# Performance work log

Measured on AMD Instinct MI355X. Metric: run time of the kernel, lower is better.

The kernel has to match this reference:

```python
import jax, jax.numpy as jnp
import numpy as np

IN_DIM = 128
SLOT_SIZE = 64
NUM_SLOTS = 8
NUM_ITERS = 3
MLP_HDIM = 128
EPSILON = 1e-08


def _layernorm(x, g, b, eps=1e-5):
    m = jnp.mean(x, axis=-1, keepdims=True)
    v = jnp.mean((x - m) ** 2, axis=-1, keepdims=True)
    return (x - m) * jax.lax.rsqrt(v + eps) * g + b


def setup_inputs() -> dict:
    key = jax.random.key(0)
    ks = jax.random.split(key, 16)
    H, D, K, M = SLOT_SIZE, IN_DIM, NUM_SLOTS, MLP_HDIM
    x = jax.random.normal(ks[0], (32, 4096, D), dtype=jnp.float32)
    noise = jax.random.normal(ks[1], (32, K, H), dtype=jnp.float32)
    s = lambda k, shape, fan_in: jax.random.normal(k, shape, jnp.float32) * (1.0 / np.sqrt(fan_in))
    return {
        'x': x,
        'noise': noise,
        'Wq': s(ks[2], (H, H), H),            # project_q (no bias)
        'Wk': s(ks[3], (H, D), D),            # project_k
        'Wv': s(ks[4], (H, D), D),            # project_v
        'ln_in_g': jnp.ones((D,), jnp.float32), 'ln_in_b': jnp.zeros((D,), jnp.float32),
        'ln_sl_g': jnp.ones((H,), jnp.float32), 'ln_sl_b': jnp.zeros((H,), jnp.float32),
        'ln_mlp_g': jnp.ones((H,), jnp.float32), 'ln_mlp_b': jnp.zeros((H,), jnp.float32),
        'gru_w_ih': s(ks[5], (3 * H, H), H),  # PyTorch GRUCell weight_ih (r,z,n)
        'gru_w_hh': s(ks[6], (3 * H, H), H),
        'gru_b_ih': jnp.zeros((3 * H,), jnp.float32),
        'gru_b_hh': jnp.zeros((3 * H,), jnp.float32),
        'mlp_w1': s(ks[7], (M, H), H), 'mlp_b1': jnp.zeros((M,), jnp.float32),
        'mlp_w2': s(ks[8], (H, M), M), 'mlp_b2': jnp.zeros((H,), jnp.float32),
        'slots_mu': jnp.tile(jnp.linspace(-1.0, 1.0, K, dtype=jnp.float32)[None, :, None], (1, 1, H)),
        'slots_logsigma': jnp.full((1, K, H), -1.0, dtype=jnp.float32),
    }


def reference(x, noise, Wq, Wk, Wv, ln_in_g, ln_in_b, ln_sl_g, ln_sl_b,
              ln_mlp_g, ln_mlp_b, gru_w_ih, gru_w_hh, gru_b_ih, gru_b_hh,
              mlp_w1, mlp_b1, mlp_w2, mlp_b2, slots_mu, slots_logsigma):
    B = x.shape[0]
    H, K = SLOT_SIZE, NUM_SLOTS
    xn = _layernorm(x, ln_in_g, ln_in_b)
    k = jnp.einsum('bnd,hd->bnh', xn, Wk)  # [B,N,H]
    v = jnp.einsum('bnd,hd->bnh', xn, Wv)

    scale = jax.nn.softplus(slots_logsigma) + 1e-05
    slots = slots_mu + scale * noise  # rsample, broadcast over batch -> [B,K,H]

    def step(slots):
        slots_prev = slots
        s = _layernorm(slots, ln_sl_g, ln_sl_b)
        q = jnp.einsum('bkh,gh->bkg', s, Wq)  # [B,K,H]
        scores = (H ** -0.5) * jnp.einsum('bnh,bkh->bnk', k, q)
        attn = jax.nn.softmax(scores, axis=-1) + EPSILON  # softmax over slots
        attn = attn / jnp.sum(attn, axis=1, keepdims=True)  # normalize over inputs
        updates = jnp.einsum('bnk,bnh->bkh', attn, v)
        # PyTorch GRUCell: gates ordered (r, z, n)
        u = updates.reshape(-1, H)
        h = slots_prev.reshape(-1, H)
        gx = u @ gru_w_ih.T + gru_b_ih
        gh = h @ gru_w_hh.T + gru_b_hh
        xr, xz, xn_ = jnp.split(gx, 3, axis=-1)
        hr, hz, hn = jnp.split(gh, 3, axis=-1)
        r = jax.nn.sigmoid(xr + hr)
        z = jax.nn.sigmoid(xz + hz)
        n = jnp.tanh(xn_ + r * hn)
        slots = ((1.0 - z) * n + z * h).reshape(B, K, H)
        slots = _layernorm(slots, ln_mlp_g, ln_mlp_b)
        mlp_out = jax.nn.relu(slots @ mlp_w1.T + mlp_b1) @ mlp_w2.T + mlp_b2
        return slots + mlp_out

    for _ in range(NUM_ITERS):
        slots = step(slots)
    return slots
```

## Files before the change

### kernel.cpp

```cpp
#include <hip/hip_runtime.h>

typedef __attribute__((ext_vector_type(8))) short s16x8;
typedef __attribute__((ext_vector_type(4))) float f32x4;

#define DEV static __device__ __forceinline__

DEV float b2f(unsigned short u){
  unsigned int i = ((unsigned int)u) << 16;
  float f; __builtin_memcpy(&f, &i, 4); return f;
}
DEV unsigned short f2b(float f){
  unsigned int i; __builtin_memcpy(&i, &f, 4);
  i = i + 0x7fffu + ((i >> 16) & 1u);
  return (unsigned short)(i >> 16);
}
DEV f32x4 mfma16(s16x8 a, s16x8 b, f32x4 c){
  return __builtin_amdgcn_mfma_f32_16x16x32_bf16(a, b, c, 0, 0, 0);
}
DEV s16x8 ld8f(const float* p){
  const float4* q4 = (const float4*)p;
  float4 a = q4[0], b = q4[1];
  s16x8 r;
  r[0]=(short)f2b(a.x); r[1]=(short)f2b(a.y); r[2]=(short)f2b(a.z); r[3]=(short)f2b(a.w);
  r[4]=(short)f2b(b.x); r[5]=(short)f2b(b.y); r[6]=(short)f2b(b.z); r[7]=(short)f2b(b.w);
  return r;
}

template<int C> DEV float dpp_addstep(float x){
  int y = __builtin_amdgcn_update_dpp(0, __builtin_bit_cast(int, x), C, 0xF, 0xF, true);
  return x + __builtin_bit_cast(float, y);
}
DEV float rsum16(float v){
  v = dpp_addstep<0xB1>(v);
  v = dpp_addstep<0x4E>(v);
  v = dpp_addstep<0x141>(v);
  v = dpp_addstep<0x140>(v);
  return v;
}

__global__ __launch_bounds__(256) void k_wpack(
    const float* __restrict__ Wk, const float* __restrict__ Wv,
    const float* __restrict__ wih, const float* __restrict__ whh,
    const float* __restrict__ w1, const float* __restrict__ w2,
    const float* __restrict__ Wq,
    unsigned short* __restrict__ wkb, unsigned short* __restrict__ wvb,
    unsigned short* __restrict__ wall)
{
  int t = blockIdx.x * 256 + threadIdx.x;
  int off = t * 4;
  const float* src; unsigned short* dst;
  if      (off <  8192){ src = Wk  + off;         dst = wkb  + off; }
  else if (off < 16384){ src = Wv  + off -  8192; dst = wvb  + off - 8192; }
  else if (off < 28672){ src = wih + off - 16384; dst = wall + off - 16384; }
  else if (off < 40960){ src = whh + off - 28672; dst = wall + off - 16384; }
  else if (off < 49152){ src = w1  + off - 40960; dst = wall + off - 16384; }
  else if (off < 57344){ src = w2  + off - 49152; dst = wall + off - 16384; }
  else                 { src = Wq  + off - 57344; dst = wall + off - 16384; }
  float4 v = *(const float4*)src;
  ushort4 o;
  o.x = f2b(v.x); o.y = f2b(v.y); o.z = f2b(v.z); o.w = f2b(v.w);
  *(ushort4*)dst = o;
}

__global__ __launch_bounds__(256, 4) void k_lnkv(
    const float* __restrict__ x,
    const unsigned short* __restrict__ wkb,
    const unsigned short* __restrict__ wvb,
    const float* __restrict__ lg,
    const float* __restrict__ lb,
    unsigned short* __restrict__ kg,
    unsigned short* __restrict__ vt)
{
  __shared__ unsigned int xs[128 * 68];
  const int tid = threadIdx.x;
  const int w = tid >> 6, ln = tid & 63;
  const int m16 = ln & 15, q = ln >> 4;
  const int b = blockIdx.x >> 5;
  const int nbase = (blockIdx.x & 31) << 7;
  const long rowg0 = (long)b * 4096 + nbase;

  {
    const int c = m16;
    const float4 gA = *(const float4*)(lg + c*4);
    const float4 gB = *(const float4*)(lg + 64 + c*4);
    const float4 bA = *(const float4*)(lb + c*4);
    const float4 bB = *(const float4*)(lb + 64 + c*4);
    const float* base = x + (rowg0 + w*32 + q)*128;

    float4 va[2], vb[2];
    va[0] = *(const float4*)(base + c*4);
    vb[0] = *(const float4*)(base + 64 + c*4);
    #pragma unroll
    for (int p = 0; p < 8; ++p){
      const int cur = p & 1, nxt = cur ^ 1;
      if (p < 7){
        va[nxt] = *(const float4*)(base + (p+1)*512 + c*4);
        vb[nxt] = *(const float4*)(base + (p+1)*512 + 64 + c*4);
      }
      float4 u = va[cur], t = vb[cur];
      float s1 = (u.x + u.y) + (u.z + u.w) + (t.x + t.y) + (t.z + t.w);
      float s2 = (u.x*u.x + u.y*u.y) + (u.z*u.z + u.w*u.w)
               + (t.x*t.x + t.y*t.y) + (t.z*t.z + t.w*t.w);
      s1 = rsum16(s1);
      s2 = rsum16(s2);
      float mean = s1 * (1.f/128.f);
      float var  = s2 * (1.f/128.f) - mean*mean;
      float rs = rsqrtf(var + 1e-5f);
      float y0 = (u.x - mean)*rs*gA.x + bA.x;
      float y1 = (u.y - mean)*rs*gA.y + bA.y;
      float y2 = (u.z - mean)*rs*gA.z + bA.z;
      float y3 = (u.w - mean)*rs*gA.w + bA.w;
      float y4 = (t.x - mean)*rs*gB.x + bB.x;
      float y5 = (t.y - mean)*rs*gB.y + bB.y;
      float y6 = (t.z - mean)*rs*gB.z + bB.z;
      float y7 = (t.w - mean)*rs*gB.w + bB.w;
      uint2 pkA, pkB;
      pkA.x = (unsigned int)f2b(y0) | ((unsigned int)f2b(y1) << 16);
      pkA.y = (unsigned int)f2b(y2) | ((unsigned int)f2b(y3) << 16);
      pkB.x = (unsigned int)f2b(y4) | ((unsigned int)f2b(y5) << 16);
      pkB.y = (unsigned int)f2b(y6) | ((unsigned int)f2b(y7) << 16);
      const int r = w*32 + p*4 + q;
      *(uint2*)&xs[r*68 + c*2] = pkA;
      *(uint2*)&xs[r*68 + 32 + c*2] = pkB;
    }
  }

  s16x8 bw[4][4];
  #pragma unroll
  for (int t = 0; t < 4; ++t)
    #pragma unroll
    for (int kb = 0; kb < 4; ++kb)
      bw[kb][t] = *(const s16x8*)(wkb + (t*16 + m16)*128 + kb*32 + q*8);

  __syncthreads();

  const f32x4 zf = {0.f, 0.f, 0.f, 0.f};

  #pragma unroll
  for (int mi = 0; mi < 2; ++mi){
    int n0 = (w*2 + mi) * 16;
    f32x4 acc[4];
    #pragma unroll
    for (int t = 0; t < 4; ++t) acc[t] = zf;
    #pragma unroll
    for (int kb = 0; kb < 4; ++kb){
      s16x8 af = *(const s16x8*)((const unsigned short*)(xs + (n0 + m16)*68) + kb*32 + q*8);
      #pragma unroll
      for (int t = 0; t < 4; ++t)
        acc[t] = mfma16(af, bw[kb][t], acc[t]);
    }
    #pragma unroll
    for (int t = 0; t < 4; ++t){
      int h = t*16 + m16;
      #pragma unroll
      for (int rr = 0; rr < 4; ++rr){
        long n = rowg0 + n0 + q*4 + rr;
        kg[n*64 + h] = f2b(acc[t][rr]);
      }
    }
  }

  #pragma unroll
  for (int t = 0; t < 4; ++t)
    #pragma unroll
    for (int kb = 0; kb < 4; ++kb)
      bw[kb][t] = *(const s16x8*)(wvb + (t*16 + m16)*128 + kb*32 + q*8);

  #pragma unroll
  for (int mi = 0; mi < 2; ++mi){
    int n0 = (w*2 + mi) * 16;
    f32x4 acc[4];
    #pragma unroll
    for (int t = 0; t < 4; ++t) acc[t] = zf;
    #pragma unroll
    for (int kb = 0; kb < 4; ++kb){
      s16x8 af = *(const s16x8*)((const unsigned short*)(xs + (n0 + m16)*68) + kb*32 + q*8);
      #pragma unroll
      for (int t = 0; t < 4; ++t)
        acc[t] = mfma16(af, bw[kb][t], acc[t]);
    }
    #pragma unroll
    for (int t = 0; t < 4; ++t){
      int h = t*16 + m16;
      unsigned int p0 = (unsigned int)f2b(acc[t][0]) | ((unsigned int)f2b(acc[t][1]) << 16);
      unsigned int p1 = (unsigned int)f2b(acc[t][2]) | ((unsigned int)f2b(acc[t][3]) << 16);
      uint2 pv; pv.x = p0; pv.y = p1;
      long off = ((long)b*64 + h)*4096 + nbase + n0 + q*4;
      *(uint2*)(vt + off) = pv;
    }
  }
}

__global__ __launch_bounds__(256) void k_init2(
    const float* __restrict__ noise,
    const float* __restrict__ mu,
    const float* __restrict__ lsg,
    const float* __restrict__ gsl,
    const float* __restrict__ bsl,
    const float* __restrict__ Wq,
    float* __restrict__ slots,
    unsigned short* __restrict__ qws,
    float* __restrict__ U0, float* __restrict__ U1, float* __restrict__ U2,
    float* __restrict__ S0, float* __restrict__ S1, float* __restrict__ S2)
{
  __shared__ unsigned short st[16*72];
  __shared__ __align__(16) float redS[16][4];
  __shared__ __align__(16) float redQ[16][4];
  const int tid = threadIdx.x;
  const int w = tid >> 6, ln = tid & 63;
  const int m16 = ln & 15, q = ln >> 4;
  const int r0 = blockIdx.x * 16;
  const int cw = w*16 + m16;

  float sl[4], s1[4], s2[4];
  #pragma unroll
  for (int rr = 0; rr < 4; ++rr){
    int row = r0 + q*4 + rr;
    int k = row & 7;
    float v = mu[k*64 + cw] + (log1pf(expf(lsg[k*64 + cw])) + 1e-5f) * noise[row*64 + cw];
    sl[rr] = v;
    slots[row*64 + cw] = v;
    s1[rr] = v; s2[rr] = v*v;
  }
  #pragma unroll
  for (int m = 1; m < 16; m <<= 1){
    #pragma unroll
    for (int rr = 0; rr < 4; ++rr){
      s1[rr] += __shfl_xor(s1[rr], m);
      s2[rr] += __shfl_xor(s2[rr], m);
    }
  }
  if (m16 == 0){
    #pragma unroll
    for (int rr = 0; rr < 4; ++rr){ redS[q*4+rr][w] = s1[rr]; redQ[q*4+rr][w] = s2[rr]; }
  }
  __syncthreads();
  {
    const float gs = gsl[cw], bs = bsl[cw];
    #pragma unroll
    for (int rr = 0; rr < 4; ++rr){
      f32x4 aS = *(const f32x4*)redS[q*4+rr];
      f32x4 aQ = *(const f32x4*)redQ[q*4+rr];
      float tS = aS[0]+aS[1]+aS[2]+aS[3];
      float tQ = aQ[0]+aQ[1]+aQ[2]+aQ[3];
      float mean = tS*(1.f/64.f);
      float var  = tQ*(1.f/64.f) - mean*mean;
      float rs = rsqrtf(var + 1e-5f);
      float sq = (sl[rr] - mean)*rs*gs + bs;
      st[(q*4+rr)*72 + cw] = f2b(sq);
    }
  }
  __syncthreads();
  {
    f32x4 acc = {0,0,0,0};
    #pragma unroll
    for (int ks = 0; ks < 2; ++ks){
      s16x8 a = *(const s16x8*)(st + m16*72 + ks*32 + q*8);
      acc = mfma16(a, ld8f(Wq + cw*64 + ks*32 + q*8), acc);
    }
    #pragma unroll
    for (int rr = 0; rr < 4; ++rr){
      int row = r0 + q*4 + rr;
      int bb_ = row >> 3, kk = row & 7;
      qws[(bb_*16 + kk)*64 + cw] = f2b(acc[rr] * 0.125f);
    }
  }
  {
    f32x4 z = {0,0,0,0};
    *(f32x4*)(U0 + r0*64 + tid*4) = z;
    *(f32x4*)(U1 + r0*64 + tid*4) = z;
    *(f32x4*)(U2 + r0*64 + tid*4) = z;
    if (tid < 16){ S0[r0 + tid] = 0.f; S1[r0 + tid] = 0.f; S2[r0 + tid] = 0.f; }
    int b0 = blockIdx.x * 2;
    ((unsigned int*)(qws + (b0*16 + 8)*64))[tid] = 0u;
    ((unsigned int*)(qws + ((b0+1)*16 + 8)*64))[tid] = 0u;
  }
}

__global__ __launch_bounds__(256) void k_attn2(
    const unsigned short* __restrict__ kg,
    const unsigned short* __restrict__ vt,
    const unsigned short* __restrict__ qws,
    const unsigned short* __restrict__ wall,
    const float* __restrict__ bih, const float* __restrict__ bhh,
    const float* __restrict__ b1p, const float* __restrict__ b2p,
    const float* __restrict__ gmlp, const float* __restrict__ bmlp,
    const float* __restrict__ gsl, const float* __restrict__ bsl,
    const float* __restrict__ Uin, const float* __restrict__ Sin,
    float* __restrict__ Uout, float* __restrict__ Sout,
    const float* __restrict__ slin, float* __restrict__ slout,
    int it)
{
  __shared__ float sc[256*17];
  __shared__ unsigned short aT[16*264];
  __shared__ unsigned short ut[16*72], ht[16*72], st[16*72], hid[16*136];
  __shared__ unsigned short qloc[16*72];
  __shared__ __align__(16) float redS[16][4];
  __shared__ __align__(16) float redQ[16][4];

  const int tid = threadIdx.x;
  const int w = tid >> 6, ln = tid & 63;
  const int m16 = ln & 15, q = ln >> 4;
  const int b = blockIdx.x >> 4;
  const int nbase = (blockIdx.x & 15) << 8;

  for (int i = tid; i < 8*264; i += 256) aT[8*264 + i] = 0;
  if (tid < 128){
    int row = 8 + (tid >> 4), c = (tid & 15)*4;
    ushort4 z4 = {0,0,0,0};
    *(ushort4*)&qloc[row*72 + c] = z4;
  }

  if (it == 0){
    if (tid < 128){
      int row = tid >> 4, c = (tid & 15)*4;
      *(ushort4*)&qloc[row*72 + c] = *(const ushort4*)(qws + (b*16 + row)*64 + c);
    }
  } else {
    const int r0 = (b >> 1) * 16;
    const int cw = w*16 + m16;
    const unsigned short* wihb = wall;
    const unsigned short* whhb = wall + 12288;
    const unsigned short* w1b  = wall + 24576;
    const unsigned short* w2b  = wall + 32768;
    const unsigned short* wqb  = wall + 40960;

    #pragma unroll
    for (int p = 0; p < 4; ++p){
      int row = p*4 + w;
      float sv = Sin[r0 + row];
      float uu = Uin[(r0 + row)*64 + ln] / sv;
      ut[row*72 + ln] = f2b(uu);
      ht[row*72 + ln] = f2b(slin[(r0 + row)*64 + ln]);
    }
    __syncthreads();

    f32x4 axr = {0,0,0,0}, axz = {0,0,0,0}, axn = {0,0,0,0};
    f32x4 ahr = {0,0,0,0}, ahz = {0,0,0,0}, ahn = {0,0,0,0};
    #pragma unroll
    for (int ks = 0; ks < 2; ++ks){
      s16x8 au = *(const s16x8*)(ut + m16*72 + ks*32 + q*8);
      s16x8 ah = *(const s16x8*)(ht + m16*72 + ks*32 + q*8);
      axr = mfma16(au, *(const s16x8*)(wihb + (      cw)*64 + ks*32 + q*8), axr);
      axz = mfma16(au, *(const s16x8*)(wihb + ( 64 + cw)*64 + ks*32 + q*8), axz);
      axn = mfma16(au, *(const s16x8*)(wihb + (128 + cw)*64 + ks*32 + q*8), axn);
      ahr = mfma16(ah, *(const s16x8*)(whhb + (      cw)*64 + ks*32 + q*8), ahr);
      ahz = mfma16(ah, *(const s16x8*)(whhb + ( 64 + cw)*64 + ks*32 + q*8), ahz);
      ahn = mfma16(ah, *(const s16x8*)(whhb + (128 + cw)*64 + ks*32 + q*8), ahn);
    }
    const float bxr = bih[cw], bxz = bih[64+cw], bxn = bih[128+cw];
    const float bhr = bhh[cw], bhz = bhh[64+cw], bhn = bhh[128+cw];
    float sp[4];
    #pragma unroll
    for (int rr = 0; rr < 4; ++rr){
      float xr = axr[rr] + bxr, xz = axz[rr] + bxz, xnv = axn[rr] + bxn;
      float hr = ahr[rr] + bhr, hz = ahz[rr] + bhz, hn = ahn[rr] + bhn;
      float rg = 1.f / (1.f + expf(-(xr + hr)));
      float zg = 1.f / (1.f + expf(-(xz + hz)));
      float ng = tanhf(xnv + rg*hn);
      float hv = b2f(ht[(q*4 + rr)*72 + cw]);
      sp[rr] = (1.f - zg)*ng + zg*hv;
    }

    float s1[4], s2[4];
    #pragma unroll
    for (int rr = 0; rr < 4; ++rr){ s1[rr] = sp[rr]; s2[rr] = sp[rr]*sp[rr]; }
    #pragma unroll
    for (int m = 1; m < 16; m <<= 1){
      #pragma unroll
      for (int rr = 0; rr < 4; ++rr){
        s1[rr] += __shfl_xor(s1[rr], m);
        s2[rr] += __shfl_xor(s2[rr], m);
      }
    }
    if (m16 == 0){
      #pragma unroll
      for (int rr = 0; rr < 4; ++rr){ redS[q*4+rr][w] = s1[rr]; redQ[q*4+rr][w] = s2[rr]; }
    }
    __syncthreads();
    float sl_[4];
    {
      const float gm = gmlp[cw], bm = bmlp[cw];
      #pragma unroll
      for (int rr = 0; rr < 4; ++rr){
        f32x4 aS = *(const f32x4*)redS[q*4+rr];
        f32x4 aQ = *(const f32x4*)redQ[q*4+rr];
        float tS = aS[0]+aS[1]+aS[2]+aS[3];
        float tQ = aQ[0]+aQ[1]+aQ[2]+aQ[3];
        float mean = tS*(1.f/64.f);
        float var  = tQ*(1.f/64.f) - mean*mean;
        float rs = rsqrtf(var + 1e-5f);
        sl_[rr] = (sp[rr] - mean)*rs*gm + bm;
        st[(q*4+rr)*72 + cw] = f2b(sl_[rr]);
      }
    }
    __syncthreads();

    #pragma unroll
    for (int t2 = 0; t2 < 2; ++t2){
      int nt = w*2 + t2;
      int col = nt*16 + m16;
      f32x4 acc = {0,0,0,0};
      #pragma unroll
      for (int ks = 0; ks < 2; ++ks){
        s16x8 a = *(const s16x8*)(st + m16*72 + ks*32 + q*8);
        acc = mfma16(a, *(const s16x8*)(w1b + col*64 + ks*32 + q*8), acc);
      }
      float bb = b1p[col];
      #pragma unroll
      for (int rr = 0; rr < 4; ++rr)
        hid[(q*4+rr)*136 + col] = f2b(fmaxf(acc[rr] + bb, 0.f));
    }
    __syncthreads();

    float snew[4];
    {
      f32x4 acc = {0,0,0,0};
      #pragma unroll
      for (int ks = 0; ks < 4; ++ks){
        s16x8 a = *(const s16x8*)(hid + m16*136 + ks*32 + q*8);
        acc = mfma16(a, *(const s16x8*)(w2b + cw*128 + ks*32 + q*8), acc);
      }
      float bb = b2p[cw];
      #pragma unroll
      for (int rr = 0; rr < 4; ++rr){
        snew[rr] = sl_[rr] + acc[rr] + bb;
        if ((blockIdx.x & 31) == 0)
          slout[(r0 + q*4 + rr)*64 + cw] = snew[rr];
      }
    }

    #pragma unroll
    for (int rr = 0; rr < 4; ++rr){ s1[rr] = snew[rr]; s2[rr] = snew[rr]*snew[rr]; }
    #pragma unroll
    for (int m = 1; m < 16; m <<= 1){
      #pragma unroll
      for (int rr = 0; rr < 4; ++rr){
        s1[rr] += __shfl_xor(s1[rr], m);
        s2[rr] += __shfl_xor(s2[rr], m);
      }
    }
    __syncthreads();
    if (m16 == 0){
      #pragma unroll
      for (int rr = 0; rr < 4; ++rr){ redS[q*4+rr][w] = s1[rr]; redQ[q*4+rr][w] = s2[rr]; }
    }
    __syncthreads();
    {
      const float gs = gsl[cw], bs = bsl[cw];
      #pragma unroll
      for (int rr = 0; rr < 4; ++rr){
        f32x4 aS = *(const f32x4*)redS[q*4+rr];
        f32x4 aQ = *(const f32x4*)redQ[q*4+rr];
        float tS = aS[0]+aS[1]+aS[2]+aS[3];
        float tQ = aQ[0]+aQ[1]+aQ[2]+aQ[3];
        float mean = tS*(1.f/64.f);
        float var  = tQ*(1.f/64.f) - mean*mean;
        float rs = rsqrtf(var + 1e-5f);
        float sq = (snew[rr] - mean)*rs*gs + bs;
        st[(q*4+rr)*72 + cw] = f2b(sq);
      }
    }
    __syncthreads();
    {
      f32x4 acc = {0,0,0,0};
      #pragma unroll
      for (int ks = 0; ks < 2; ++ks){
        s16x8 a = *(const s16x8*)(st + m16*72 + ks*32 + q*8);
        acc = mfma16(a, *(const s16x8*)(wqb + cw*64 + ks*32 + q*8), acc);
      }
      #pragma unroll
      for (int rr = 0; rr < 4; ++rr){
        int rloc = q*4 + rr;
        if ((rloc >> 3) == (b & 1))
          qloc[(rloc & 7)*72 + cw] = f2b(acc[rr] * 0.125f);
      }
    }
  }
  __syncthreads();

  s16x8 bq[2];
  #pragma unroll
  for (int ks = 0; ks < 2; ++ks)
    bq[ks] = *(const s16x8*)(qloc + m16*72 + ks*32 + q*8);

  #pragma unroll
  for (int mi = 0; mi < 4; ++mi){
    int n0 = (w*4 + mi)*16;
    f32x4 acc = {0.f, 0.f, 0.f, 0.f};
    #pragma unroll
    for (int ks = 0; ks < 2; ++ks){
      s16x8 af = *(const s16x8*)(kg + ((long)b*4096 + nbase + n0 + m16)*64 + ks*32 + q*8);
      acc = mfma16(af, bq[ks], acc);
    }
    #pragma unroll
    for (int rr = 0; rr < 4; ++rr)
      sc[(n0 + q*4 + rr)*17 + m16] = acc[rr];
  }
  __syncthreads();

  {
    int r = tid;
    float a8[8];
    float mx = -1e30f;
    #pragma unroll
    for (int j = 0; j < 8; ++j){ a8[j] = sc[r*17 + j]; mx = fmaxf(mx, a8[j]); }
    float ssum = 0.f;
    #pragma unroll
    for (int j = 0; j < 8; ++j){ a8[j] = expf(a8[j] - mx); ssum += a8[j]; }
    float inv = 1.f/ssum;
    #pragma unroll
    for (int j = 0; j < 8; ++j)
      aT[j*264 + r] = f2b(a8[j]*inv + 1e-8f);
  }
  __syncthreads();

  {
    int j = tid >> 5, c = tid & 31;
    float p = 0.f;
    #pragma unroll
    for (int i = 0; i < 8; ++i) p += b2f(aT[j*264 + c + 32*i]);
    #pragma unroll
    for (int m = 16; m >= 1; m >>= 1) p += __shfl_xor(p, m);
    if ((ln & 31) == 0) atomicAdd(&Sout[b*8 + j], p);
  }

  {
    f32x4 acc = {0.f, 0.f, 0.f, 0.f};
    #pragma unroll
    for (int ks = 0; ks < 8; ++ks){
      s16x8 af = *(const s16x8*)(aT + m16*264 + ks*32 + q*8);
      s16x8 bf = *(const s16x8*)(vt + ((long)b*64 + w*16 + m16)*4096 + nbase + ks*32 + q*8);
      acc = mfma16(af, bf, acc);
    }
    #pragma unroll
    for (int rr = 0; rr < 4; ++rr){
      int slot = q*4 + rr;
      if (slot < 8)
        atomicAdd(&Uout[b*512 + slot*64 + w*16 + m16], acc[rr]);
    }
  }
}

__global__ __launch_bounds__(256) void k_gru(
    const float* __restrict__ U, const float* __restrict__ S,
    float* __restrict__ slots,
    const float* __restrict__ wih, const float* __restrict__ whh,
    const float* __restrict__ bih, const float* __restrict__ bhh,
    const float* __restrict__ w1, const float* __restrict__ b1p,
    const float* __restrict__ w2, const float* __restrict__ b2p,
    const float* __restrict__ gmlp, const float* __restrict__ bmlp,
    float* __restrict__ outp)
{
  __shared__ unsigned short ut[16*72], ht[16*72], st[16*72], hid[16*136];
  __shared__ __align__(16) float redS[16][4];
  __shared__ __align__(16) float redQ[16][4];
  const int tid = threadIdx.x;
  const int w = tid >> 6, ln = tid & 63;
  const int m16 = ln & 15, q = ln >> 4;
  const int r0 = blockIdx.x * 16;
  const int cw = w*16 + m16;

  #pragma unroll
  for (int p = 0; p < 4; ++p){
    int row = p*4 + w;
    float sv = S[r0 + row];
    float uu = U[(r0 + row)*64 + ln] / sv;
    ut[row*72 + ln] = f2b(uu);
    ht[row*72 + ln] = f2b(slots[(r0 + row)*64 + ln]);
  }
  __syncthreads();

  f32x4 axr = {0,0,0,0}, axz = {0,0,0,0}, axn = {0,0,0,0};
  f32x4 ahr = {0,0,0,0}, ahz = {0,0,0,0}, ahn = {0,0,0,0};
  #pragma unroll
  for (int ks = 0; ks < 2; ++ks){
    s16x8 au = *(const s16x8*)(ut + m16*72 + ks*32 + q*8);
    s16x8 ah = *(const s16x8*)(ht + m16*72 + ks*32 + q*8);
    axr = mfma16(au, ld8f(wih + (      cw)*64 + ks*32 + q*8), axr);
    axz = mfma16(au, ld8f(wih + ( 64 + cw)*64 + ks*32 + q*8), axz);
    axn = mfma16(au, ld8f(wih + (128 + cw)*64 + ks*32 + q*8), axn);
    ahr = mfma16(ah, ld8f(whh + (      cw)*64 + ks*32 + q*8), ahr);
    ahz = mfma16(ah, ld8f(whh + ( 64 + cw)*64 + ks*32 + q*8), ahz);
    ahn = mfma16(ah, ld8f(whh + (128 + cw)*64 + ks*32 + q*8), ahn);
  }
  const float bxr = bih[cw], bxz = bih[64+cw], bxn = bih[128+cw];
  const float bhr = bhh[cw], bhz = bhh[64+cw], bhn = bhh[128+cw];
  float sp[4];
  #pragma unroll
  for (int rr = 0; rr < 4; ++rr){
    float xr = axr[rr] + bxr, xz = axz[rr] + bxz, xnv = axn[rr] + bxn;
    float hr = ahr[rr] + bhr, hz = ahz[rr] + bhz, hn = ahn[rr] + bhn;
    float rg = 1.f / (1.f + expf(-(xr + hr)));
    float zg = 1.f / (1.f + expf(-(xz + hz)));
    float ng = tanhf(xnv + rg*hn);
    float hv = b2f(ht[(q*4 + rr)*72 + cw]);
    sp[rr] = (1.f - zg)*ng + zg*hv;
  }

  float s1[4], s2[4];
  #pragma unroll
  for (int rr = 0; rr < 4; ++rr){ s1[rr] = sp[rr]; s2[rr] = sp[rr]*sp[rr]; }
  #pragma unroll
  for (int m = 1; m < 16; m <<= 1){
    #pragma unroll
    for (int rr = 0; rr < 4; ++rr){
      s1[rr] += __shfl_xor(s1[rr], m);
      s2[rr] += __shfl_xor(s2[rr], m);
    }
  }
  if (m16 == 0){
    #pragma unroll
    for (int rr = 0; rr < 4; ++rr){ redS[q*4+rr][w] = s1[rr]; redQ[q*4+rr][w] = s2[rr]; }
  }
  __syncthreads();
  float sl_[4];
  {
    const float gm = gmlp[cw], bm = bmlp[cw];
    #pragma unroll
    for (int rr = 0; rr < 4; ++rr){
      f32x4 aS = *(const f32x4*)redS[q*4+rr];
      f32x4 aQ = *(const f32x4*)redQ[q*4+rr];
      float tS = aS[0]+aS[1]+aS[2]+aS[3];
      float tQ = aQ[0]+aQ[1]+aQ[2]+aQ[3];
      float mean = tS*(1.f/64.f);
      float var  = tQ*(1.f/64.f) - mean*mean;
      float rs = rsqrtf(var + 1e-5f);
      sl_[rr] = (sp[rr] - mean)*rs*gm + bm;
      st[(q*4+rr)*72 + cw] = f2b(sl_[rr]);
    }
  }
  __syncthreads();

  #pragma unroll
  for (int t2 = 0; t2 < 2; ++t2){
    int nt = w*2 + t2;
    int col = nt*16 + m16;
    f32x4 acc = {0,0,0,0};
    #pragma unroll
    for (int ks = 0; ks < 2; ++ks){
      s16x8 a = *(const s16x8*)(st + m16*72 + ks*32 + q*8);
      acc = mfma16(a, ld8f(w1 + col*64 + ks*32 + q*8), acc);
    }
    float bb = b1p[col];
    #pragma unroll
    for (int rr = 0; rr < 4; ++rr)
      hid[(q*4+rr)*136 + col] = f2b(fmaxf(acc[rr] + bb, 0.f));
  }
  __syncthreads();

  {
    f32x4 acc = {0,0,0,0};
    #pragma unroll
    for (int ks = 0; ks < 4; ++ks){
      s16x8 a = *(const s16x8*)(hid + m16*136 + ks*32 + q*8);
      acc = mfma16(a, ld8f(w2 + cw*128 + ks*32 + q*8), acc);
    }
    float bb = b2p[cw];
    #pragma unroll
    for (int rr = 0; rr < 4; ++rr){
      int row = r0 + q*4 + rr;
      outp[row*64 + cw] = sl_[rr] + acc[rr] + bb;
    }
  }
}

extern "C" void kernel_launch(void* const* d_in, const int* in_sizes, int n_in,
                              void* d_out, int out_size, void* d_ws, size_t ws_size,
                              hipStream_t stream)
{
  const float* x    = (const float*)d_in[0];
  const float* noise= (const float*)d_in[1];
  const float* Wq   = (const float*)d_in[2];
  const float* Wk   = (const float*)d_in[3];
  const float* Wv   = (const float*)d_in[4];
  const float* ling = (const float*)d_in[5];
  const float* linb = (const float*)d_in[6];
  const float* gsl  = (const float*)d_in[7];
  const float* bsl  = (const float*)d_in[8];
  const float* gmlp = (const float*)d_in[9];
  const float* bmlp = (const float*)d_in[10];
  const float* wih  = (const float*)d_in[11];
  const float* whh  = (const float*)d_in[12];
  const float* bih  = (const float*)d_in[13];
  const float* bhh  = (const float*)d_in[14];
  const float* w1   = (const float*)d_in[15];
  const float* b1p  = (const float*)d_in[16];
  const float* w2   = (const float*)d_in[17];
  const float* b2p  = (const float*)d_in[18];
  const float* mu   = (const float*)d_in[19];
  const float* lsg  = (const float*)d_in[20];

  char* ws = (char*)d_ws;
  unsigned short* kg   = (unsigned short*)(ws);
  unsigned short* vt   = (unsigned short*)(ws + 16777216);
  char* base = ws + 33554432;
  unsigned short* qws  = (unsigned short*)(base);
  float* slotsA        = (float*)(base + 65536);
  float* slotsB        = (float*)(base + 131072);
  float* slotsC        = (float*)(base + 196608);
  float* U0            = (float*)(base + 262144);
  float* U1            = (float*)(base + 327680);
  float* U2            = (float*)(base + 393216);
  float* S0            = (float*)(base + 458752);
  float* S1            = (float*)(base + 459776);
  float* S2            = (float*)(base + 460800);
  unsigned short* wkb  = (unsigned short*)(base + 461824);
  unsigned short* wvb  = (unsigned short*)(base + 478208);
  unsigned short* wall = (unsigned short*)(base + 494592);
  float* outp          = (float*)d_out;

  hipLaunchKernelGGL(k_wpack, dim3(60), dim3(256), 0, stream,
                     Wk, Wv, wih, whh, w1, w2, Wq, wkb, wvb, wall);
  hipLaunchKernelGGL(k_lnkv, dim3(1024), dim3(256), 0, stream, x, wkb, wvb, ling, linb, kg, vt);
  hipLaunchKernelGGL(k_init2, dim3(16), dim3(256), 0, stream,
                     noise, mu, lsg, gsl, bsl, Wq, slotsA, qws, U0, U1, U2, S0, S1, S2);
  hipLaunchKernelGGL(k_attn2, dim3(512), dim3(256), 0, stream,
                     kg, vt, qws, wall, bih, bhh, b1p, b2p, gmlp, bmlp, gsl, bsl,
                     U0, S0, U0, S0, slotsA, slotsA, 0);
  hipLaunchKernelGGL(k_attn2, dim3(512), dim3(256), 0, stream,
                     kg, vt, qws, wall, bih, bhh, b1p, b2p, gmlp, bmlp, gsl, bsl,
                     U0, S0, U1, S1, slotsA, slotsB, 1);
  hipLaunchKernelGGL(k_attn2, dim3(512), dim3(256), 0, stream,
                     kg, vt, qws, wall, bih, bhh, b1p, b2p, gmlp, bmlp, gsl, bsl,
                     U1, S1, U2, S2, slotsB, slotsC, 2);
  hipLaunchKernelGGL(k_gru, dim3(16), dim3(256), 0, stream, U2, S2, slotsC,
                     wih, whh, bih, bhh, w1, b1p, w2, b2p, gmlp, bmlp, outp);
  (void)in_sizes; (void)n_in; (void)out_size; (void)ws_size;
}
```

Before: 209.2 us.

## Replace atomic accumulation with per-tile partials and fold slot init into LN kernel

The attention kernel now writes per-tile partial update sums and normalizers to separate slots instead of using global atomicAdd. The next stage reduces the 16 partials itself, so the U/S buffers no longer need zeroing. The slot-init/query work is appended as extra blocks of the layernorm K/V kernel, which removes one kernel launch. The cost is extra partial-buffer traffic and a 16-way reduction in each consumer, while atomic contention goes away.

```diff
diff --git a/kernel.cpp b/kernel.cpp
--- a/kernel.cpp
+++ b/kernel.cpp
@@ -62,19 +62,95 @@
   *(ushort4*)dst = o;
 }
 
-__global__ __launch_bounds__(256, 4) void k_lnkv(
+__global__ __launch_bounds__(256, 4) void k_lnkv5(
     const float* __restrict__ x,
     const unsigned short* __restrict__ wkb,
     const unsigned short* __restrict__ wvb,
     const float* __restrict__ lg,
     const float* __restrict__ lb,
     unsigned short* __restrict__ kg,
-    unsigned short* __restrict__ vt)
+    unsigned short* __restrict__ vt,
+    const float* __restrict__ noise,
+    const float* __restrict__ mu,
+    const float* __restrict__ lsg,
+    const float* __restrict__ gsl,
+    const float* __restrict__ bsl,
+    const float* __restrict__ Wq,
+    float* __restrict__ slots,
+    unsigned short* __restrict__ qws)
 {
-  __shared__ unsigned int xs[128 * 68];
+  __shared__ __align__(16) unsigned int xs[128 * 68];
   const int tid = threadIdx.x;
   const int w = tid >> 6, ln = tid & 63;
   const int m16 = ln & 15, q = ln >> 4;
+
+  if (blockIdx.x >= 1024){
+    unsigned short* st = (unsigned short*)xs;
+    float (*redS)[4] = (float(*)[4])((char*)xs + 2304);
+    float (*redQ)[4] = (float(*)[4])((char*)xs + 2560);
+    const int bi = blockIdx.x - 1024;
+    const int r0 = bi * 16;
+    const int cw = w*16 + m16;
+
+    float sl[4], s1[4], s2[4];
+    #pragma unroll
+    for (int rr = 0; rr < 4; ++rr){
+      int row = r0 + q*4 + rr;
+      int k = row & 7;
+      float v = mu[k*64 + cw] + (log1pf(expf(lsg[k*64 + cw])) + 1e-5f) * noise[row*64 + cw];
+      sl[rr] = v;
+      slots[row*64 + cw] = v;
+      s1[rr] = v; s2[rr] = v*v;
+    }
+    #pragma unroll
+    for (int m = 1; m < 16; m <<= 1){
+      #pragma unroll
+      for (int rr = 0; rr < 4; ++rr){
+        s1[rr] += __shfl_xor(s1[rr], m);
+        s2[rr] += __shfl_xor(s2[rr], m);
+      }
+    }
+    if (m16 == 0){
+      #pragma unroll
+      for (int rr = 0; rr < 4; ++rr){ redS[q*4+rr][w] = s1[rr]; redQ[q*4+rr][w] = s2[rr]; }
+    }
+    __syncthreads();
+    {
+      const float gs = gsl[cw], bs = bsl[cw];
+      #pragma unroll
+      for (int rr = 0; rr < 4; ++rr){
+        f32x4 aS = *(const f32x4*)redS[q*4+rr];
+        f32x4 aQ = *(const f32x4*)redQ[q*4+rr];
+        float tS = aS[0]+aS[1]+aS[2]+aS[3];
+        float tQ = aQ[0]+aQ[1]+aQ[2]+aQ[3];
+        float mean = tS*(1.f/64.f);
+        float var  = tQ*(1.f/64.f) - mean*mean;
+        float rs = rsqrtf(var + 1e-5f);
+        float sq = (sl[rr] - mean)*rs*gs + bs;
+        st[(q*4+rr)*72 + cw] = f2b(sq);
+      }
+    }
+    __syncthreads();
+    {
+      f32x4 acc = {0,0,0,0};
+      #pragma unroll
+      for (int ks = 0; ks < 2; ++ks){
+        s16x8 a = *(const s16x8*)(st + m16*72 + ks*32 + q*8);
+        acc = mfma16(a, ld8f(Wq + cw*64 + ks*32 + q*8), acc);
+      }
+      #pragma unroll
+      for (int rr = 0; rr < 4; ++rr){
+        int row = r0 + q*4 + rr;
+        int bb_ = row >> 3, kk = row & 7;
+        qws[(bb_*16 + kk)*64 + cw] = f2b(acc[rr] * 0.125f);
+      }
+      int b0 = bi * 2;
+      ((unsigned int*)(qws + (b0*16 + 8)*64))[tid] = 0u;
+      ((unsigned int*)(qws + ((b0+1)*16 + 8)*64))[tid] = 0u;
+    }
+    return;
+  }
+
   const int b = blockIdx.x >> 5;
   const int nbase = (blockIdx.x & 31) << 7;
   const long rowg0 = (long)b * 4096 + nbase;
@@ -191,93 +267,7 @@
   }
 }
 
-__global__ __launch_bounds__(256) void k_init2(
-    const float* __restrict__ noise,
-    const float* __restrict__ mu,
-    const float* __restrict__ lsg,
-    const float* __restrict__ gsl,
-    const float* __restrict__ bsl,
-    const float* __restrict__ Wq,
-    float* __restrict__ slots,
-    unsigned short* __restrict__ qws,
-    float* __restrict__ U0, float* __restrict__ U1, float* __restrict__ U2,
-    float* __restrict__ S0, float* __restrict__ S1, float* __restrict__ S2)
-{
-  __shared__ unsigned short st[16*72];
-  __shared__ __align__(16) float redS[16][4];
-  __shared__ __align__(16) float redQ[16][4];
-  const int tid = threadIdx.x;
-  const int w = tid >> 6, ln = tid & 63;
-  const int m16 = ln & 15, q = ln >> 4;
-  const int r0 = blockIdx.x * 16;
-  const int cw = w*16 + m16;
-
-  float sl[4], s1[4], s2[4];
-  #pragma unroll
-  for (int rr = 0; rr < 4; ++rr){
-    int row = r0 + q*4 + rr;
-    int k = row & 7;
-    float v = mu[k*64 + cw] + (log1pf(expf(lsg[k*64 + cw])) + 1e-5f) * noise[row*64 + cw];
-    sl[rr] = v;
-    slots[row*64 + cw] = v;
-    s1[rr] = v; s2[rr] = v*v;
-  }
-  #pragma unroll
-  for (int m = 1; m < 16; m <<= 1){
-    #pragma unroll
-    for (int rr = 0; rr < 4; ++rr){
-      s1[rr] += __shfl_xor(s1[rr], m);
-      s2[rr] += __shfl_xor(s2[rr], m);
-    }
-  }
-  if (m16 == 0){
-    #pragma unroll
-    for (int rr = 0; rr < 4; ++rr){ redS[q*4+rr][w] = s1[rr]; redQ[q*4+rr][w] = s2[rr]; }
-  }
-  __syncthreads();
-  {
-    const float gs = gsl[cw], bs = bsl[cw];
-    #pragma unroll
-    for (int rr = 0; rr < 4; ++rr){
-      f32x4 aS = *(const f32x4*)redS[q*4+rr];
-      f32x4 aQ = *(const f32x4*)redQ[q*4+rr];
-      float tS = aS[0]+aS[1]+aS[2]+aS[3];
-      float tQ = aQ[0]+aQ[1]+aQ[2]+aQ[3];
-      float mean = tS*(1.f/64.f);
-      float var  = tQ*(1.f/64.f) - mean*mean;
-      float rs = rsqrtf(var + 1e-5f);
-      float sq = (sl[rr] - mean)*rs*gs + bs;
-      st[(q*4+rr)*72 + cw] = f2b(sq);
-    }
-  }
-  __syncthreads();
-  {
-    f32x4 acc = {0,0,0,0};
-    #pragma unroll
-    for (int ks = 0; ks < 2; ++ks){
-      s16x8 a = *(const s16x8*)(st + m16*72 + ks*32 + q*8);
-      acc = mfma16(a, ld8f(Wq + cw*64 + ks*32 + q*8), acc);
-    }
-    #pragma unroll
-    for (int rr = 0; rr < 4; ++rr){
-      int row = r0 + q*4 + rr;
-      int bb_ = row >> 3, kk = row & 7;
-      qws[(bb_*16 + kk)*64 + cw] = f2b(acc[rr] * 0.125f);
-    }
-  }
-  {
-    f32x4 z = {0,0,0,0};
-    *(f32x4*)(U0 + r0*64 + tid*4) = z;
-    *(f32x4*)(U1 + r0*64 + tid*4) = z;
-    *(f32x4*)(U2 + r0*64 + tid*4) = z;
-    if (tid < 16){ S0[r0 + tid] = 0.f; S1[r0 + tid] = 0.f; S2[r0 + tid] = 0.f; }
-    int b0 = blockIdx.x * 2;
-    ((unsigned int*)(qws + (b0*16 + 8)*64))[tid] = 0u;
-    ((unsigned int*)(qws + ((b0+1)*16 + 8)*64))[tid] = 0u;
-  }
-}
-
-__global__ __launch_bounds__(256) void k_attn2(
+__global__ __launch_bounds__(256) void k_attn3(
     const unsigned short* __restrict__ kg,
     const unsigned short* __restrict__ vt,
     const unsigned short* __restrict__ qws,
@@ -286,8 +276,8 @@
     const float* __restrict__ b1p, const float* __restrict__ b2p,
     const float* __restrict__ gmlp, const float* __restrict__ bmlp,
     const float* __restrict__ gsl, const float* __restrict__ bsl,
-    const float* __restrict__ Uin, const float* __restrict__ Sin,
-    float* __restrict__ Uout, float* __restrict__ Sout,
+    const float* __restrict__ Up_in, const float* __restrict__ Sp_in,
+    float* __restrict__ Up_out, float* __restrict__ Sp_out,
     const float* __restrict__ slin, float* __restrict__ slout,
     int it)
 {
@@ -302,7 +292,8 @@
   const int w = tid >> 6, ln = tid & 63;
   const int m16 = ln & 15, q = ln >> 4;
   const int b = blockIdx.x >> 4;
-  const int nbase = (blockIdx.x & 15) << 8;
+  const int tile = blockIdx.x & 15;
+  const int nbase = tile << 8;
 
   for (int i = tid; i < 8*264; i += 256) aT[8*264 + i] = 0;
   if (tid < 128){
@@ -328,10 +319,18 @@
     #pragma unroll
     for (int p = 0; p < 4; ++p){
       int row = p*4 + w;
-      float sv = Sin[r0 + row];
-      float uu = Uin[(r0 + row)*64 + ln] / sv;
-      ut[row*72 + ln] = f2b(uu);
-      ht[row*72 + ln] = f2b(slin[(r0 + row)*64 + ln]);
+      int g = r0 + row;
+      int bb = g >> 3, sl = g & 7;
+      const float* up  = Up_in + ((bb*16)*8 + sl)*64 + ln;
+      const float* spp = Sp_in + (bb*16)*8 + sl;
+      float usum = 0.f, ssum = 0.f;
+      #pragma unroll
+      for (int t = 0; t < 16; ++t){
+        usum += up[t*512];
+        ssum += spp[t*8];
+      }
+      ut[row*72 + ln] = f2b(usum / ssum);
+      ht[row*72 + ln] = f2b(slin[g*64 + ln]);
     }
     __syncthreads();
 
@@ -522,7 +521,7 @@
     for (int i = 0; i < 8; ++i) p += b2f(aT[j*264 + c + 32*i]);
     #pragma unroll
     for (int m = 16; m >= 1; m >>= 1) p += __shfl_xor(p, m);
-    if ((ln & 31) == 0) atomicAdd(&Sout[b*8 + j], p);
+    if ((tid & 31) == 0) Sp_out[(b*16 + tile)*8 + j] = p;
   }
 
   {
@@ -533,18 +532,19 @@
       s16x8 bf = *(const s16x8*)(vt + ((long)b*64 + w*16 + m16)*4096 + nbase + ks*32 + q*8);
       acc = mfma16(af, bf, acc);
     }
+    float* ub = Up_out + ((b*16 + tile)*8)*64 + w*16 + m16;
     #pragma unroll
     for (int rr = 0; rr < 4; ++rr){
       int slot = q*4 + rr;
       if (slot < 8)
-        atomicAdd(&Uout[b*512 + slot*64 + w*16 + m16], acc[rr]);
-    }
-  }
-}
-
-__global__ __launch_bounds__(256) void k_gru(
-    const float* __restrict__ U, const float* __restrict__ S,
-    float* __restrict__ slots,
+        ub[slot*64] = acc[rr];
+    }
+  }
+}
+
+__global__ __launch_bounds__(256) void k_gru2(
+    const float* __restrict__ Up, const float* __restrict__ Sp,
+    const float* __restrict__ slots,
     const float* __restrict__ wih, const float* __restrict__ whh,
     const float* __restrict__ bih, const float* __restrict__ bhh,
     const float* __restrict__ w1, const float* __restrict__ b1p,
@@ -564,10 +564,18 @@
   #pragma unroll
   for (int p = 0; p < 4; ++p){
     int row = p*4 + w;
-    float sv = S[r0 + row];
-    float uu = U[(r0 + row)*64 + ln] / sv;
-    ut[row*72 + ln] = f2b(uu);
-    ht[row*72 + ln] = f2b(slots[(r0 + row)*64 + ln]);
+    int g = r0 + row;
+    int bb = g >> 3, sl = g & 7;
+    const float* up  = Up + ((bb*16)*8 + sl)*64 + ln;
+    const float* spp = Sp + (bb*16)*8 + sl;
+    float usum = 0.f, ssum = 0.f;
+    #pragma unroll
+    for (int t = 0; t < 16; ++t){
+      usum += up[t*512];
+      ssum += spp[t*8];
+    }
+    ut[row*72 + ln] = f2b(usum / ssum);
+    ht[row*72 + ln] = f2b(slots[g*64 + ln]);
   }
   __syncthreads();
 
@@ -699,32 +707,30 @@
   float* slotsA        = (float*)(base + 65536);
   float* slotsB        = (float*)(base + 131072);
   float* slotsC        = (float*)(base + 196608);
-  float* U0            = (float*)(base + 262144);
-  float* U1            = (float*)(base + 327680);
-  float* U2            = (float*)(base + 393216);
-  float* S0            = (float*)(base + 458752);
-  float* S1            = (float*)(base + 459776);
-  float* S2            = (float*)(base + 460800);
-  unsigned short* wkb  = (unsigned short*)(base + 461824);
-  unsigned short* wvb  = (unsigned short*)(base + 478208);
-  unsigned short* wall = (unsigned short*)(base + 494592);
+  float* UA            = (float*)(base + 262144);
+  float* UB            = (float*)(base + 1310720);
+  float* SA            = (float*)(base + 2359296);
+  float* SB            = (float*)(base + 2375680);
+  unsigned short* wkb  = (unsigned short*)(base + 2392064);
+  unsigned short* wvb  = (unsigned short*)(base + 2408448);
+  unsigned short* wall = (unsigned short*)(base + 2424832);
   float* outp          = (float*)d_out;
 
   hipLaunchKernelGGL(k_wpack, dim3(60), dim3(256), 0, stream,
                      Wk, Wv, wih, whh, w1, w2, Wq, wkb, wvb, wall);
-  hipLaunchKernelGGL(k_lnkv, dim3(1024), dim3(256), 0, stream, x, wkb, wvb, ling, linb, kg, vt);
-  hipLaunchKernelGGL(k_init2, dim3(16), dim3(256), 0, stream,
-                     noise, mu, lsg, gsl, bsl, Wq, slotsA, qws, U0, U1, U2, S0, S1, S2);
-  hipLaunchKernelGGL(k_attn2, dim3(512), dim3(256), 0, stream,
+  hipLaunchKernelGGL(k_lnkv5, dim3(1040), dim3(256), 0, stream,
+                     x, wkb, wvb, ling, linb, kg, vt,
+                     noise, mu, lsg, gsl, bsl, Wq, slotsA, qws);
+  hipLaunchKernelGGL(k_attn3, dim3(512), dim3(256), 0, stream,
                      kg, vt, qws, wall, bih, bhh, b1p, b2p, gmlp, bmlp, gsl, bsl,
-                     U0, S0, U0, S0, slotsA, slotsA, 0);
-  hipLaunchKernelGGL(k_attn2, dim3(512), dim3(256), 0, stream,
+                     UA, SA, UA, SA, slotsA, slotsA, 0);
+  hipLaunchKernelGGL(k_attn3, dim3(512), dim3(256), 0, stream,
                      kg, vt, qws, wall, bih, bhh, b1p, b2p, gmlp, bmlp, gsl, bsl,
-                     U0, S0, U1, S1, slotsA, slotsB, 1);
-  hipLaunchKernelGGL(k_attn2, dim3(512), dim3(256), 0, stream,
+                     UA, SA, UB, SB, slotsA, slotsB, 1);
+  hipLaunchKernelGGL(k_attn3, dim3(512), dim3(256), 0, stream,
                      kg, vt, qws, wall, bih, bhh, b1p, b2p, gmlp, bmlp, gsl, bsl,
-                     U1, S1, U2, S2, slotsB, slotsC, 2);
-  hipLaunchKernelGGL(k_gru, dim3(16), dim3(256), 0, stream, U2, S2, slotsC,
+                     UB, SB, UA, SA, slotsB, slotsC, 2);
+  hipLaunchKernelGGL(k_gru2, dim3(16), dim3(256), 0, stream, UA, SA, slotsC,
                      wih, whh, bih, bhh, w1, b1p, w2, b2p, gmlp, bmlp, outp);
   (void)in_sizes; (void)n_in; (void)out_size; (void)ws_size;
 }
```

Result: faster. 203.2 us (-2.8%).
